# Optimization experiments

Hardware: AMD Instinct MI355X
Metric: run time of the kernel (lower is better)

The kernel has to match this reference:

```python
import jax, jax.numpy as jnp
import numpy as np

B, L, C, H = 8, 2048, 256, 4
D = C // H  # head_dim = 64
EPS = 1e-5


def setup_inputs() -> dict:
    key = jax.random.key(0)
    ks = jax.random.split(key, 16)
    s = lambda fan_in: 1.0 / np.sqrt(fan_in)
    inp = {
        'x0': jax.random.normal(ks[0], (B, L, C), jnp.float32),
        'x1': jax.random.normal(ks[1], (B, L, C), jnp.float32),
        # attention projections (stored as (in, out); torch Linear is x @ W.T + b)
        'Wqk': jax.random.normal(ks[2], (C, C), jnp.float32) * s(C),
        'bqk': jax.random.normal(ks[3], (C,), jnp.float32) * s(C),
        'Wv': jax.random.normal(ks[4], (C, C), jnp.float32) * s(C),
        'bv': jax.random.normal(ks[5], (C,), jnp.float32) * s(C),
        'Wout': jax.random.normal(ks[6], (C, C), jnp.float32) * s(C),
        'bout': jax.random.normal(ks[7], (C,), jnp.float32) * s(C),
        # shared FFN: Linear(2C->2C) -> LayerNorm -> GELU -> Linear(2C->C)
        'W1': jax.random.normal(ks[8], (2 * C, 2 * C), jnp.float32) * s(2 * C),
        'b1': jax.random.normal(ks[9], (2 * C,), jnp.float32) * s(2 * C),
        'ln_g': jnp.ones((2 * C,), jnp.float32),
        'ln_b': jnp.zeros((2 * C,), jnp.float32),
        'W2': jax.random.normal(ks[10], (2 * C, C), jnp.float32) * s(2 * C),
        'b2': jax.random.normal(ks[11], (C,), jnp.float32) * s(2 * C),
    }
    return inp


def _heads(t):
    # (B, L, C) -> (B, H, L, D)
    b, l, _ = t.shape
    return t.reshape(b, l, H, D).transpose(0, 2, 1, 3)


def _merge(t):
    # (B, H, L, D) -> (B, L, C)
    b, h, l, d = t.shape
    return t.transpose(0, 2, 1, 3).reshape(b, l, h * d)


def _ffn(z, W1, b1, ln_g, ln_b, W2, b2):
    h = z @ W1 + b1
    mu = jnp.mean(h, axis=-1, keepdims=True)
    var = jnp.var(h, axis=-1, keepdims=True)
    h = (h - mu) * jax.lax.rsqrt(var + EPS) * ln_g + ln_b
    h = jax.nn.gelu(h, approximate=False)
    return h @ W2 + b2


def reference(x0, x1, Wqk, bqk, Wv, bv, Wout, bout, W1, b1, ln_g, ln_b, W2, b2):
    scale_sqrt = D ** (-0.25)  # sqrt(head_dim**-0.5), applied to both sides
    qk0 = _heads(x0 @ Wqk + bqk) * scale_sqrt  # (B,H,M,D)
    qk1 = _heads(x1 @ Wqk + bqk) * scale_sqrt  # (B,H,N,D)
    v0 = _heads(x0 @ Wv + bv)
    v1 = _heads(x1 @ Wv + bv)

    # single shared similarity matrix (LightGlue trick)
    sim = jnp.einsum('bhid,bhjd->bhij', qk0, qk1)  # (B,H,M,N)
    attn01 = jax.nn.softmax(sim, axis=-1)           # rows: A->B
    attn10 = jax.nn.softmax(sim, axis=-2)           # cols: B->A (softmax of sim^T along last dim)
    m0 = jnp.einsum('bhij,bhjd->bhid', attn01, v1)  # (B,H,M,D)
    m1 = jnp.einsum('bhij,bhid->bhjd', attn10, v0)  # (B,H,N,D)

    m0 = _merge(m0) @ Wout + bout
    m1 = _merge(m1) @ Wout + bout

    x0_out = x0 + _ffn(jnp.concatenate([x0, m0], axis=-1), W1, b1, ln_g, ln_b, W2, b2)
    x1_out = x1 + _ffn(jnp.concatenate([x1, m1], axis=-1), W1, b1, ln_g, ln_b, W2, b2)
    return (x0_out, x1_out)
```

## Files before the change

### kernel.cpp

```cpp
#include <hip/hip_runtime.h>
#include <hip/hip_bf16.h>

typedef _Float16 f16;
typedef _Float16 f16x8 __attribute__((ext_vector_type(8)));
typedef _Float16 f16x4 __attribute__((ext_vector_type(4)));
typedef _Float16 f16x2 __attribute__((ext_vector_type(2)));
typedef float f32x4 __attribute__((ext_vector_type(4)));

#define MFMA16(a, b, c) __builtin_amdgcn_mfma_f32_16x16x32_f16((a), (b), (c), 0, 0, 0)

__device__ __forceinline__ void load16(const void* g, void* l) {
    __builtin_amdgcn_global_load_lds((const __attribute__((address_space(1))) void*)g,
                                     (__attribute__((address_space(3))) void*)l, 16, 0, 0);
}

__device__ __forceinline__ unsigned int pkrtz(float a, float b) {
    return __builtin_bit_cast(unsigned int, __builtin_amdgcn_cvt_pkrtz(a, b));
}

__global__ __launch_bounds__(256) void k_prep(const float* __restrict__ x0,
                                              const float* __restrict__ x1,
                                              const float* __restrict__ Wqk,
                                              const float* __restrict__ Wv,
                                              const float* __restrict__ W1,
                                              const float* __restrict__ W2,
                                              const float* __restrict__ Wout,
                                              const float* __restrict__ b1,
                                              const float* __restrict__ bout,
                                              f16* __restrict__ xh, f16* __restrict__ wcat_t,
                                              f16* __restrict__ w1t, f16* __restrict__ w1bt,
                                              f16* __restrict__ w2t, f16* __restrict__ woutf16,
                                              float* __restrict__ bias_eff) {
    __shared__ float red[4];
    const int blk = blockIdx.x, tid = threadIdx.x;
    if (blk < 8192) {
        size_t i = ((size_t)blk * 256 + tid) * 4;
        const float* src = (i < 4194304) ? (x0 + i) : (x1 + (i - 4194304));
        float4 v = *(const float4*)src;
        f16x4 o = {(f16)v.x, (f16)v.y, (f16)v.z, (f16)v.w};
        *(f16x4*)(xh + i) = o;
    } else if (blk < 8704) {
        int n = blk - 8192;
        const float* W = (n < 256) ? Wqk : Wv;
        wcat_t[n * 256 + tid] = (f16)W[tid * 256 + (n & 255)];
    } else if (blk < 9216) {
        int n = blk - 8704;
        w1t[n * 512 + tid] = (f16)W1[tid * 512 + n];
    } else if (blk < 9728) {
        int n = blk - 9216;
        w1bt[n * 256 + tid] = (f16)W1[(256 + tid) * 512 + n];
    } else if (blk < 10240) {
        int j = blk - 9728;
        int n = j >> 1, k = (j & 1) * 256 + tid;
        w2t[n * 512 + k] = (f16)W2[k * 256 + n];
    } else if (blk < 10496) {
        int o = (blk - 10240) * 256 + tid;
        woutf16[o] = (f16)Wout[o];
    } else {
        int n = blk - 10496;
        float s = bout[tid] * W1[(size_t)(256 + tid) * 512 + n];
#pragma unroll
        for (int off = 1; off < 64; off <<= 1) s += __shfl_xor(s, off);
        int wave = tid >> 6, lane = tid & 63;
        if (lane == 0) red[wave] = s;
        __syncthreads();
        if (tid == 0) bias_eff[n] = b1[n] + red[0] + red[1] + red[2] + red[3];
    }
}

template <int TM>
__global__ __launch_bounds__(256, 2) void k_gemm(const f16* __restrict__ A1,
                                                 const f16* __restrict__ A2, int ksplit,
                                                 int strideA, const f16* __restrict__ Bt, int K,
                                                 int N, const float* __restrict__ bias1,
                                                 const float* __restrict__ bias2, int mode,
                                                 void* __restrict__ out1, void* __restrict__ out2,
                                                 const f16* __restrict__ resh,
                                                 const f16* __restrict__ pgA,
                                                 const f16* __restrict__ pgBt,
                                                 f16* __restrict__ pgOut) {
    constexpr int WM = TM / 2;
    constexpr int TMI = WM / 16;
    constexpr int ARD = TM / 64;
    int bm0 = blockIdx.x * TM;
    int bn0 = blockIdx.y * 256;
    if constexpr (TM == 128) {
        if (pgOut != nullptr && blockIdx.x >= 256) {
            if (blockIdx.y != 0) return;
            A1 = pgA;
            A2 = pgA;
            ksplit = 1 << 30;
            strideA = 256;
            Bt = pgBt;
            K = 256;
            N = 256;
            bias1 = nullptr;
            bias2 = nullptr;
            mode = 4;
            out1 = pgOut;
            out2 = nullptr;
            resh = nullptr;
            bm0 = (blockIdx.x - 256) * 128;
            bn0 = 0;
        }
    }
    __shared__ f16 As[2][TM * 32];
    __shared__ f16 Bs[2][8192];
    const int tid = threadIdx.x;
    const int lane = tid & 63, wave = tid >> 6;
    const int quad = lane >> 4, l16 = lane & 15;
    const int wm0 = (wave & 1) * WM, wn0 = (wave >> 1) * 128;
    const int axor = l16 & 3;

    f32x4 acc[TMI][8];
#pragma unroll
    for (int tm = 0; tm < TMI; tm++)
#pragma unroll
        for (int tn = 0; tn < 8; tn++) acc[tm][tn] = (f32x4){0.f, 0.f, 0.f, 0.f};

    auto stage = [&](int buf, int kt) {
        const int k0 = kt * 32;
        const f16* Ab = (k0 < ksplit) ? A1 : A2;
        const int koff = (k0 < ksplit) ? k0 : k0 - ksplit;
#pragma unroll
        for (int rd = 0; rd < ARD; rd++) {
            const int cbase = rd * 256 + wave * 64;
            const int c = cbase + lane;
            const int row = c >> 2, col = (c & 3) ^ (row & 3);
            load16(Ab + (size_t)(bm0 + row) * strideA + koff + col * 8, &As[buf][cbase * 8]);
        }
#pragma unroll
        for (int rd = 0; rd < 4; rd++) {
            const int cbase = rd * 256 + wave * 64;
            const int c = cbase + lane;
            const int row = c >> 2, col = (c & 3) ^ (row & 3);
            load16(Bt + (size_t)(bn0 + row) * K + k0 + col * 8, &Bs[buf][cbase * 8]);
        }
    };

    const int NT = K >> 5;
    stage(0, 0);
    for (int kt = 0; kt < NT; kt++) {
        const int cur = kt & 1;
        if (kt + 1 < NT) {
            stage(cur ^ 1, kt + 1);
            if constexpr (TM == 128)
                asm volatile("s_waitcnt vmcnt(6)" ::: "memory");
            else
                asm volatile("s_waitcnt vmcnt(5)" ::: "memory");
        } else {
            asm volatile("s_waitcnt vmcnt(0)" ::: "memory");
        }
        __builtin_amdgcn_s_barrier();
        f16x8 af[TMI], bf[8];
#pragma unroll
        for (int t = 0; t < TMI; t++)
            af[t] = *(const f16x8*)&As[cur][(wm0 + t * 16 + l16) * 32 + (quad ^ axor) * 8];
#pragma unroll
        for (int t = 0; t < 8; t++)
            bf[t] = *(const f16x8*)&Bs[cur][(wn0 + t * 16 + l16) * 32 + (quad ^ axor) * 8];
#pragma unroll
        for (int tm = 0; tm < TMI; tm++)
#pragma unroll
            for (int tn = 0; tn < 8; tn++) acc[tm][tn] = MFMA16(bf[tn], af[tm], acc[tm][tn]);
        __builtin_amdgcn_s_barrier();
    }

    if constexpr (TM == 128) {
        if (mode == 0 && bn0 == 0) {
            f16* tile = &Bs[0][0];
#pragma unroll
            for (int tm = 0; tm < TMI; tm++) {
                const int r = (wave & 1) * 16 + l16;
#pragma unroll
                for (int tn = 0; tn < 8; tn++) {
                    const int c = wn0 + tn * 16 + quad * 4;
                    float4 bi = *(const float4*)(bias1 + c);
                    f32x4 v = acc[tm][tn];
                    f16x4 o = {(f16)((v[0] + bi.x) * 0.42466090f),
                               (f16)((v[1] + bi.y) * 0.42466090f),
                               (f16)((v[2] + bi.z) * 0.42466090f),
                               (f16)((v[3] + bi.w) * 0.42466090f)};
                    *(f16x4*)&tile[r * 264 + c] = o;
                }
                __syncthreads();
#pragma unroll
                for (int j = 0; j < 4; j++) {
                    const int ch = tid + j * 256;
                    const int row = ch >> 5, cc = (ch & 31) * 8;
                    const int m = bm0 + (row >> 4) * WM + tm * 16 + (row & 15);
                    const int s = m >> 14, r14 = m & 16383, b = r14 >> 11, l = r14 & 2047;
                    const int h = cc >> 6, d = cc & 63;
                    const size_t hh = (size_t)((s * 8 + b) * 4 + h);
                    *(f16x8*)((f16*)out1 + (hh * 2048 + l) * 64 + d) =
                        *(const f16x8*)&tile[row * 264 + cc];
                }
                __syncthreads();
            }
            return;
        }
    }

    if (mode == 2) {
        f16* tile = &Bs[0][0];
#pragma unroll
        for (int tm = 0; tm < TMI; tm++) {
            const int r = (wave & 1) * 16 + l16;
#pragma unroll
            for (int tn = 0; tn < 8; tn++) {
                const int c = wn0 + tn * 16 + quad * 4;
                float4 bi = *(const float4*)(bias1 + bn0 + c);
                f32x4 v = acc[tm][tn];
                f16x4 o = {(f16)(v[0] + bi.x), (f16)(v[1] + bi.y), (f16)(v[2] + bi.z),
                           (f16)(v[3] + bi.w)};
                *(f16x4*)&tile[r * 264 + c] = o;
            }
            __syncthreads();
#pragma unroll
            for (int j = 0; j < 4; j++) {
                const int ch = tid + j * 256;
                const int row = ch >> 5, cc = (ch & 31) * 8;
                const int m = bm0 + (row >> 4) * WM + tm * 16 + (row & 15);
                *(f16x8*)((f16*)out1 + (size_t)m * N + bn0 + cc) =
                    *(const f16x8*)&tile[row * 264 + cc];
            }
            __syncthreads();
        }
        return;
    }

    if (mode == 3) {
        float* t32 = (float*)&Bs[0][0];
#pragma unroll
        for (int tm = 0; tm < TMI; tm++) {
#pragma unroll
            for (int half = 0; half < 2; half++) {
                if ((wave & 1) == half) {
#pragma unroll
                    for (int tn = 0; tn < 8; tn++) {
                        const int c = wn0 + tn * 16 + quad * 4;
                        float4 bi = *(const float4*)(bias1 + c);
                        f32x4 v = acc[tm][tn];
                        float4 o = {v[0] + bi.x, v[1] + bi.y, v[2] + bi.z, v[3] + bi.w};
                        *(float4*)&t32[l16 * 264 + c] = o;
                    }
                }
                __syncthreads();
#pragma unroll
                for (int j = 0; j < 4; j++) {
                    const int ch = tid + j * 256;
                    const int row = ch >> 6, cc = (ch & 63) * 4;
                    const int m = bm0 + half * WM + tm * 16 + row;
                    f16x4 rr = *(const f16x4*)(resh + (size_t)m * 256 + cc);
                    const float* ts = &t32[row * 264 + cc];
                    float4 o = {ts[0] + (float)rr[0], ts[1] + (float)rr[1],
                                ts[2] + (float)rr[2], ts[3] + (float)rr[3]};
                    *(float4*)((float*)out1 + (size_t)m * 256 + cc) = o;
                }
                __syncthreads();
            }
        }
        return;
    }

    if constexpr (TM == 128) {
#pragma unroll
        for (int tm = 0; tm < TMI; tm++) {
            const int m = bm0 + wm0 + tm * 16 + l16;
#pragma unroll
            for (int tn = 0; tn < 8; tn++) {
                const int n = bn0 + wn0 + tn * 16 + quad * 4;
                f32x4 v = acc[tm][tn];
                if (mode == 0) {
                    const int s = m >> 14, r14 = m & 16383, b = r14 >> 11, l = r14 & 2047;
                    const int n2 = n - 256;
                    float4 bi = *(const float4*)(bias2 + n2);
                    const int h = n2 >> 6, d = n2 & 63;
                    const size_t hh = (size_t)((s * 8 + b) * 4 + h);
                    f16* o2 = (f16*)out2 + (hh * 64 + d) * 2048 + l;
                    o2[0] = (f16)(v[0] + bi.x);
                    o2[2048] = (f16)(v[1] + bi.y);
                    o2[4096] = (f16)(v[2] + bi.z);
                    o2[6144] = (f16)(v[3] + bi.w);
                } else {
                    f16x4 o = {(f16)v[0], (f16)v[1], (f16)v[2], (f16)v[3]};
                    *(f16x4*)((f16*)out1 + (size_t)m * 512 + 256 + n) = o;
                }
            }
        }
    }
}

__global__ __launch_bounds__(256, 4) void k_flash(const f16* __restrict__ qkbuf,
                                                  const f16* __restrict__ vtbuf,
                                                  f16* __restrict__ mbuf) {
    const int z = blockIdx.z;
    const int bh = blockIdx.x;
    const int qt = blockIdx.y;
    const size_t HSZ = 2048 * 64;
    const size_t SSZ = 32 * HSZ;
    const f16* Q = qkbuf + (z ? SSZ : 0) + bh * HSZ;
    const f16* Kp = qkbuf + (z ? 0 : SSZ) + bh * HSZ;
    const f16* Vt = vtbuf + (z ? 0 : SSZ) + bh * HSZ;
    f16* Mo = mbuf + (size_t)z * (16384 * 256);

    __shared__ f16 Ks[2][4096];
    __shared__ f16 Vs[2][4096];

    const int tid = threadIdx.x, lane = tid & 63, wave = tid >> 6;
    const int quad = lane >> 4, l16 = lane & 15;
    const int srow = lane >> 3;
    const int slc = (lane & 7) ^ (srow & 7);
    const int sw = l16 & 7;

    const int q0 = qt * 128 + wave * 32;
    f16x8 qf[2][2];
#pragma unroll
    for (int tq = 0; tq < 2; tq++)
#pragma unroll
        for (int kk = 0; kk < 2; kk++)
            qf[tq][kk] =
                *(const f16x8*)(Q + (size_t)(q0 + tq * 16 + l16) * 64 + kk * 32 + quad * 8);

    const f16* kb[2] = {&Ks[0][l16 * 64 + ((0 + quad) ^ sw) * 8],
                        &Ks[0][l16 * 64 + ((4 + quad) ^ sw) * 8]};
    const f16* vb[2] = {&Vs[0][l16 * 64 + ((0 + quad) ^ sw) * 8],
                        &Vs[0][l16 * 64 + ((4 + quad) ^ sw) * 8]};

    const f16* pK0 = Kp + (size_t)(wave * 16 + srow) * 64 + slc * 8;
    const f16* pK1 = pK0 + 8 * 64;
    const f16* pV0 = Vt + (size_t)(wave * 16 + srow) * 2048 + slc * 8;
    const f16* pV1 = pV0 + 8 * 2048;
    f16* kd0 = &Ks[0][(wave * 2 + 0) * 512];
    f16* kd1 = &Ks[0][(wave * 2 + 1) * 512];
    f16* vd0 = &Vs[0][(wave * 2 + 0) * 512];
    f16* vd1 = &Vs[0][(wave * 2 + 1) * 512];

    auto stage = [&](int buf, int kv0) {
        load16(pK0 + (size_t)kv0 * 64, kd0 + buf * 4096);
        load16(pK1 + (size_t)kv0 * 64, kd1 + buf * 4096);
        load16(pV0 + kv0, vd0 + buf * 4096);
        load16(pV1 + kv0, vd1 + buf * 4096);
    };

    f32x4 oacc[4][2];
#pragma unroll
    for (int td = 0; td < 4; td++)
#pragma unroll
        for (int tq = 0; tq < 2; tq++) oacc[td][tq] = (f32x4){0.f, 0.f, 0.f, 0.f};
    f32x4 oext[2] = {{0.f, 0.f, 0.f, 0.f}, {0.f, 0.f, 0.f, 0.f}};
    const f16x8 vones = {(f16)1.f, (f16)1.f, (f16)1.f, (f16)1.f,
                         (f16)1.f, (f16)1.f, (f16)1.f, (f16)1.f};
    const f32x4 nbias = {-8.f, -8.f, -8.f, -8.f};

    stage(0, 0);

    auto body = [&](int cur, int t) {
        if (t < 31) {
            stage(cur ^ 1, (t + 1) * 64);
            asm volatile("s_waitcnt vmcnt(4)" ::: "memory");
        } else {
            asm volatile("s_waitcnt vmcnt(0)" ::: "memory");
        }
        __builtin_amdgcn_s_barrier();

        f32x4 sacc[4][2];
#pragma unroll
        for (int kk = 0; kk < 2; kk++) {
#pragma unroll
            for (int tkv = 0; tkv < 4; tkv++) {
                f16x8 ka = *(const f16x8*)(kb[kk] + cur * 4096 + tkv * 1024);
#pragma unroll
                for (int tq = 0; tq < 2; tq++)
                    sacc[tkv][tq] = MFMA16(ka, qf[tq][kk], kk == 0 ? nbias : sacc[tkv][tq]);
            }
        }

        f16x8 bfrag[2][2];
#pragma unroll
        for (int blk = 0; blk < 2; blk++) {
#pragma unroll
            for (int tq = 0; tq < 2; tq++) {
                unsigned int rg[2][2];
#pragma unroll
                for (int tt = 0; tt < 2; tt++) {
                    const int tkv = blk * 2 + tt;
                    float p0 = __builtin_amdgcn_exp2f(sacc[tkv][tq][0]);
                    float p1 = __builtin_amdgcn_exp2f(sacc[tkv][tq][1]);
                    float p2 = __builtin_amdgcn_exp2f(sacc[tkv][tq][2]);
                    float p3 = __builtin_amdgcn_exp2f(sacc[tkv][tq][3]);
                    rg[tt][0] = pkrtz(p0, p1);
                    rg[tt][1] = pkrtz(p2, p3);
                }
                auto ab0 = __builtin_amdgcn_permlane32_swap(rg[0][0], rg[1][0], false, false);
                auto uw0 = __builtin_amdgcn_permlane16_swap(ab0[0], ab0[1], false, false);
                auto ab1 = __builtin_amdgcn_permlane32_swap(rg[0][1], rg[1][1], false, false);
                auto uw1 = __builtin_amdgcn_permlane16_swap(ab1[0], ab1[1], false, false);
                union {
                    unsigned int u[4];
                    f16x8 v;
                } bb;
                bb.u[0] = uw0[0];
                bb.u[1] = uw1[0];
                bb.u[2] = uw0[1];
                bb.u[3] = uw1[1];
                bfrag[blk][tq] = bb.v;
            }
        }

#pragma unroll
        for (int blk = 0; blk < 2; blk++) {
#pragma unroll
            for (int td = 0; td < 4; td++) {
                f16x8 va = *(const f16x8*)(vb[blk] + cur * 4096 + td * 1024);
#pragma unroll
                for (int tq = 0; tq < 2; tq++)
                    oacc[td][tq] = MFMA16(va, bfrag[blk][tq], oacc[td][tq]);
            }
#pragma unroll
            for (int tq = 0; tq < 2; tq++)
                oext[tq] = MFMA16(vones, bfrag[blk][tq], oext[tq]);
        }
        __builtin_amdgcn_s_barrier();
    };

    for (int t = 0; t < 32; t += 2) {
        body(0, t);
        body(1, t + 1);
    }

    const int b = bh >> 2, h = bh & 3;
#pragma unroll
    for (int tq = 0; tq < 2; tq++) {
        const float inv = 1.f / oext[tq][0];
        const int q = q0 + tq * 16 + l16;
        const size_t base = ((size_t)(b * 2048 + q)) * 256 + h * 64;
#pragma unroll
        for (int td = 0; td < 4; td++) {
            f16x4 o = {(f16)(oacc[td][tq][0] * inv), (f16)(oacc[td][tq][1] * inv),
                       (f16)(oacc[td][tq][2] * inv), (f16)(oacc[td][tq][3] * inv)};
            *(f16x4*)(Mo + base + td * 16 + quad * 4) = o;
        }
    }
}

__global__ __launch_bounds__(256) void k_ln_gelu(f16* __restrict__ h,
                                                 const float* __restrict__ g,
                                                 const float* __restrict__ bb) {
    const int tid = threadIdx.x, wave = tid >> 6, lane = tid & 63;
    const size_t row = (size_t)blockIdx.x * 4 + wave;
    f16* hr = h + row * 512 + lane * 8;
    f16x8 v = *(const f16x8*)hr;
    float x[8];
    float s = 0.f, sq = 0.f;
#pragma unroll
    for (int i = 0; i < 8; i++) {
        x[i] = (float)v[i];
        s += x[i];
        sq += x[i] * x[i];
    }
#pragma unroll
    for (int off = 1; off < 64; off <<= 1) {
        s += __shfl_xor(s, off);
        sq += __shfl_xor(sq, off);
    }
    const float mu = s * (1.f / 512.f);
    const float var = sq * (1.f / 512.f) - mu * mu;
    const float rstd = rsqrtf(var + 1e-5f);
    float4 g0 = *(const float4*)(g + lane * 8), g1 = *(const float4*)(g + lane * 8 + 4);
    float4 b0 = *(const float4*)(bb + lane * 8), b1 = *(const float4*)(bb + lane * 8 + 4);
    float gg[8] = {g0.x, g0.y, g0.z, g0.w, g1.x, g1.y, g1.z, g1.w};
    float bv[8] = {b0.x, b0.y, b0.z, b0.w, b1.x, b1.y, b1.z, b1.w};
#pragma unroll
    for (int i = 0; i < 8; i++) {
        float a = (x[i] - mu) * rstd * gg[i] + bv[i];
        a = 0.5f * a * (1.f + erff(a * 0.70710678118f));
        v[i] = (f16)a;
    }
    *(f16x8*)hr = v;
}


extern "C" void kernel_launch(void* const* d_in, const int* in_sizes, int n_in, void* d_out,
                              int out_size, void* d_ws, size_t ws_size, hipStream_t stream) {
    const float* x0 = (const float*)d_in[0];
    const float* x1 = (const float*)d_in[1];
    const float* Wqk = (const float*)d_in[2];
    const float* bqk = (const float*)d_in[3];
    const float* Wv = (const float*)d_in[4];
    const float* bv = (const float*)d_in[5];
    const float* Wout = (const float*)d_in[6];
    const float* bout = (const float*)d_in[7];
    const float* W1 = (const float*)d_in[8];
    const float* b1 = (const float*)d_in[9];
    const float* lng = (const float*)d_in[10];
    const float* lnb = (const float*)d_in[11];
    const float* W2 = (const float*)d_in[12];
    const float* b2 = (const float*)d_in[13];
    float* out = (float*)d_out;

    char* ws = (char*)d_ws;
    f16* xh = (f16*)(ws);
    f16* qk = (f16*)(ws + 16777216);
    f16* vt = (f16*)(ws + 33554432);
    f16* mbuf = (f16*)(ws + 50331648);
    f16* hbuf = qk;
    f16* w1bt = (f16*)(ws + 50331648);
    f16* woutf16 = w1bt + 131072;
    f16* wcat_t = (f16*)(ws + 67108864);
    f16* w1t = wcat_t + 131072;
    f16* w2t = w1t + 262144;
    float* bias_eff = (float*)(w2t + 131072);

    k_prep<<<11008, 256, 0, stream>>>(x0, x1, Wqk, Wv, W1, W2, Wout, b1, bout, xh, wcat_t, w1t,
                                      w1bt, w2t, woutf16, bias_eff);
    k_gemm<128><<<dim3(260, 2), 256, 0, stream>>>(xh, xh, 1 << 30, 256, wcat_t, 256, 512, bqk,
                                                  bv, 0, qk, vt, nullptr, w1bt, woutf16, w1t);
    k_flash<<<dim3(32, 16, 2), 256, 0, stream>>>(qk, vt, mbuf);
    k_gemm<64><<<dim3(512, 2), 256, 0, stream>>>(xh, mbuf, 256, 256, w1t, 512, 512, bias_eff,
                                                 nullptr, 2, hbuf, nullptr, nullptr, nullptr,
                                                 nullptr, nullptr);
    k_ln_gelu<<<8192, 256, 0, stream>>>(hbuf, lng, lnb);
    k_gemm<64><<<dim3(512, 1), 256, 0, stream>>>(hbuf, hbuf, 1 << 30, 512, w2t, 512, 256, b2,
                                                 nullptr, 3, out, nullptr, xh, nullptr, nullptr,
                                                 nullptr);
}
```

Before: 283.7 us.

## Fuse FFN first GEMM with LayerNorm and GELU into one full-row kernel

Replaces the split-N first FFN GEMM (mode 2) and the separate LayerNorm+GELU kernel with a new kernel where each block computes a 64-row by full-512-column tile. Row statistics are reduced across waves through shared memory, then normalization and exact GELU are applied before a single f16 store. This removes one full write and re-read of the 32768x512 hidden buffer and one kernel launch. In exchange, each block holds a much larger accumulator (32 MFMA tiles per wave) and streams the whole weight tile per K step, which lowers occupancy and increases per-block LDS traffic.

```diff
diff --git a/kernel.cpp b/kernel.cpp
--- a/kernel.cpp
+++ b/kernel.cpp
@@ -201,34 +201,6 @@
         }
     }
 
-    if (mode == 2) {
-        f16* tile = &Bs[0][0];
-#pragma unroll
-        for (int tm = 0; tm < TMI; tm++) {
-            const int r = (wave & 1) * 16 + l16;
-#pragma unroll
-            for (int tn = 0; tn < 8; tn++) {
-                const int c = wn0 + tn * 16 + quad * 4;
-                float4 bi = *(const float4*)(bias1 + bn0 + c);
-                f32x4 v = acc[tm][tn];
-                f16x4 o = {(f16)(v[0] + bi.x), (f16)(v[1] + bi.y), (f16)(v[2] + bi.z),
-                           (f16)(v[3] + bi.w)};
-                *(f16x4*)&tile[r * 264 + c] = o;
-            }
-            __syncthreads();
-#pragma unroll
-            for (int j = 0; j < 4; j++) {
-                const int ch = tid + j * 256;
-                const int row = ch >> 5, cc = (ch & 31) * 8;
-                const int m = bm0 + (row >> 4) * WM + tm * 16 + (row & 15);
-                *(f16x8*)((f16*)out1 + (size_t)m * N + bn0 + cc) =
-                    *(const f16x8*)&tile[row * 264 + cc];
-            }
-            __syncthreads();
-        }
-        return;
-    }
-
     if (mode == 3) {
         float* t32 = (float*)&Bs[0][0];
 #pragma unroll
@@ -288,6 +260,140 @@
                 }
             }
         }
+    }
+}
+
+__global__ __launch_bounds__(256, 2) void k_ffn1(const f16* __restrict__ A1,
+                                                 const f16* __restrict__ A2,
+                                                 const f16* __restrict__ Bt,
+                                                 const float* __restrict__ bias_eff,
+                                                 const float* __restrict__ lng,
+                                                 const float* __restrict__ lnb,
+                                                 f16* __restrict__ out) {
+    const int bm0 = blockIdx.x * 64;
+    __shared__ f16 As[2][2048];
+    __shared__ f16 Bs[2][16384];
+    __shared__ float red[2][2][16][2][2];
+    const int tid = threadIdx.x;
+    const int lane = tid & 63, wave = tid >> 6;
+    const int quad = lane >> 4, l16 = lane & 15;
+    const int mgrp = wave & 1, ngrp = wave >> 1;
+    const int wm0 = mgrp * 32, wn0 = ngrp * 256;
+    const int axor = l16 & 3;
+
+    f32x4 acc[2][16];
+#pragma unroll
+    for (int tm = 0; tm < 2; tm++)
+#pragma unroll
+        for (int tn = 0; tn < 16; tn++) acc[tm][tn] = (f32x4){0.f, 0.f, 0.f, 0.f};
+
+    auto stage = [&](int buf, int kt) {
+        const int k0 = kt * 32;
+        const f16* Ab = (k0 < 256) ? A1 : A2;
+        const int koff = (k0 < 256) ? k0 : k0 - 256;
+        {
+            const int cbase = wave * 64;
+            const int c = cbase + lane;
+            const int row = c >> 2, col = (c & 3) ^ (row & 3);
+            load16(Ab + (size_t)(bm0 + row) * 256 + koff + col * 8, &As[buf][cbase * 8]);
+        }
+#pragma unroll
+        for (int rd = 0; rd < 8; rd++) {
+            const int cbase = rd * 256 + wave * 64;
+            const int c = cbase + lane;
+            const int row = c >> 2, col = (c & 3) ^ (row & 3);
+            load16(Bt + (size_t)row * 512 + k0 + col * 8, &Bs[buf][cbase * 8]);
+        }
+    };
+
+    stage(0, 0);
+    for (int kt = 0; kt < 16; kt++) {
+        const int cur = kt & 1;
+        if (kt + 1 < 16) {
+            stage(cur ^ 1, kt + 1);
+            asm volatile("s_waitcnt vmcnt(9)" ::: "memory");
+        } else {
+            asm volatile("s_waitcnt vmcnt(0)" ::: "memory");
+        }
+        __builtin_amdgcn_s_barrier();
+        f16x8 af[2], bf[16];
+#pragma unroll
+        for (int t = 0; t < 2; t++)
+            af[t] = *(const f16x8*)&As[cur][(wm0 + t * 16 + l16) * 32 + (quad ^ axor) * 8];
+#pragma unroll
+        for (int t = 0; t < 16; t++)
+            bf[t] = *(const f16x8*)&Bs[cur][(wn0 + t * 16 + l16) * 32 + (quad ^ axor) * 8];
+#pragma unroll
+        for (int tm = 0; tm < 2; tm++)
+#pragma unroll
+            for (int tn = 0; tn < 16; tn++) acc[tm][tn] = MFMA16(bf[tn], af[tm], acc[tm][tn]);
+        __builtin_amdgcn_s_barrier();
+    }
+
+    float mu[2], rs[2];
+#pragma unroll
+    for (int tm = 0; tm < 2; tm++) {
+        float s = 0.f, sq = 0.f;
+#pragma unroll
+        for (int tn = 0; tn < 16; tn++) {
+            const int c = wn0 + tn * 16 + quad * 4;
+            float4 bi = *(const float4*)(bias_eff + c);
+            f32x4 v = acc[tm][tn];
+            v[0] += bi.x;
+            v[1] += bi.y;
+            v[2] += bi.z;
+            v[3] += bi.w;
+            acc[tm][tn] = v;
+            s += (v[0] + v[1]) + (v[2] + v[3]);
+            sq += (v[0] * v[0] + v[1] * v[1]) + (v[2] * v[2] + v[3] * v[3]);
+        }
+        s += __shfl_xor(s, 16);
+        sq += __shfl_xor(sq, 16);
+        s += __shfl_xor(s, 32);
+        sq += __shfl_xor(sq, 32);
+        if (quad == 0) {
+            red[mgrp][tm][l16][ngrp][0] = s;
+            red[mgrp][tm][l16][ngrp][1] = sq;
+        }
+    }
+    __syncthreads();
+#pragma unroll
+    for (int tm = 0; tm < 2; tm++) {
+        const float s = red[mgrp][tm][l16][0][0] + red[mgrp][tm][l16][1][0];
+        const float sq = red[mgrp][tm][l16][0][1] + red[mgrp][tm][l16][1][1];
+        mu[tm] = s * (1.f / 512.f);
+        const float var = sq * (1.f / 512.f) - mu[tm] * mu[tm];
+        rs[tm] = rsqrtf(var + 1e-5f);
+    }
+
+    f16* tile = &Bs[0][0];
+#pragma unroll
+    for (int tm = 0; tm < 2; tm++) {
+        const int r = mgrp * 16 + l16;
+#pragma unroll
+        for (int tn = 0; tn < 16; tn++) {
+            const int c = wn0 + tn * 16 + quad * 4;
+            float4 g = *(const float4*)(lng + c);
+            float4 bb = *(const float4*)(lnb + c);
+            f32x4 v = acc[tm][tn];
+            float y[4] = {(v[0] - mu[tm]) * rs[tm] * g.x + bb.x,
+                          (v[1] - mu[tm]) * rs[tm] * g.y + bb.y,
+                          (v[2] - mu[tm]) * rs[tm] * g.z + bb.z,
+                          (v[3] - mu[tm]) * rs[tm] * g.w + bb.w};
+#pragma unroll
+            for (int i = 0; i < 4; i++) y[i] = 0.5f * y[i] * (1.f + erff(y[i] * 0.70710678118f));
+            f16x4 o = {(f16)y[0], (f16)y[1], (f16)y[2], (f16)y[3]};
+            *(f16x4*)&tile[r * 520 + c] = o;
+        }
+        __syncthreads();
+#pragma unroll
+        for (int j = 0; j < 8; j++) {
+            const int ch = tid + j * 256;
+            const int row = ch >> 6, cc = (ch & 63) * 8;
+            const int m = bm0 + (row >> 4) * 32 + tm * 16 + (row & 15);
+            *(f16x8*)(out + (size_t)m * 512 + cc) = *(const f16x8*)&tile[row * 520 + cc];
+        }
+        __syncthreads();
     }
 }
 
@@ -444,42 +550,6 @@
     }
 }
 
-__global__ __launch_bounds__(256) void k_ln_gelu(f16* __restrict__ h,
-                                                 const float* __restrict__ g,
-                                                 const float* __restrict__ bb) {
-    const int tid = threadIdx.x, wave = tid >> 6, lane = tid & 63;
-    const size_t row = (size_t)blockIdx.x * 4 + wave;
-    f16* hr = h + row * 512 + lane * 8;
-    f16x8 v = *(const f16x8*)hr;
-    float x[8];
-    float s = 0.f, sq = 0.f;
-#pragma unroll
-    for (int i = 0; i < 8; i++) {
-        x[i] = (float)v[i];
-        s += x[i];
-        sq += x[i] * x[i];
-    }
-#pragma unroll
-    for (int off = 1; off < 64; off <<= 1) {
-        s += __shfl_xor(s, off);
-        sq += __shfl_xor(sq, off);
-    }
-    const float mu = s * (1.f / 512.f);
-    const float var = sq * (1.f / 512.f) - mu * mu;
-    const float rstd = rsqrtf(var + 1e-5f);
-    float4 g0 = *(const float4*)(g + lane * 8), g1 = *(const float4*)(g + lane * 8 + 4);
-    float4 b0 = *(const float4*)(bb + lane * 8), b1 = *(const float4*)(bb + lane * 8 + 4);
-    float gg[8] = {g0.x, g0.y, g0.z, g0.w, g1.x, g1.y, g1.z, g1.w};
-    float bv[8] = {b0.x, b0.y, b0.z, b0.w, b1.x, b1.y, b1.z, b1.w};
-#pragma unroll
-    for (int i = 0; i < 8; i++) {
-        float a = (x[i] - mu) * rstd * gg[i] + bv[i];
-        a = 0.5f * a * (1.f + erff(a * 0.70710678118f));
-        v[i] = (f16)a;
-    }
-    *(f16x8*)hr = v;
-}
-
 
 extern "C" void kernel_launch(void* const* d_in, const int* in_sizes, int n_in, void* d_out,
                               int out_size, void* d_ws, size_t ws_size, hipStream_t stream) {
@@ -517,10 +587,7 @@
     k_gemm<128><<<dim3(260, 2), 256, 0, stream>>>(xh, xh, 1 << 30, 256, wcat_t, 256, 512, bqk,
                                                   bv, 0, qk, vt, nullptr, w1bt, woutf16, w1t);
     k_flash<<<dim3(32, 16, 2), 256, 0, stream>>>(qk, vt, mbuf);
-    k_gemm<64><<<dim3(512, 2), 256, 0, stream>>>(xh, mbuf, 256, 256, w1t, 512, 512, bias_eff,
-                                                 nullptr, 2, hbuf, nullptr, nullptr, nullptr,
-                                                 nullptr, nullptr);
-    k_ln_gelu<<<8192, 256, 0, stream>>>(hbuf, lng, lnb);
+    k_ffn1<<<512, 256, 0, stream>>>(xh, mbuf, w1t, bias_eff, lng, lnb, hbuf);
     k_gemm<64><<<dim3(512, 1), 256, 0, stream>>>(hbuf, hbuf, 1 << 30, 512, w2t, 512, 256, b2,
                                                  nullptr, 3, out, nullptr, xh, nullptr, nullptr,
                                                  nullptr);
```

Result: slower. 298.7 us (+5.3%).
